# Kernel optimization log

Hardware: AMD Instinct MI355X
Metric: run time of the kernel (lower is better)

The kernel has to match this reference:

```python
import jax, jax.numpy as jnp
import numpy as np

NEG_SLOPE = 0.2


def gat_conv(x, src, dst, W, a_src, a_dst, b, concat):
    # x: [N, F_in], src/dst: [E], W: [F_in, H*C], a_src/a_dst: [H, C], b: [H*C] or [C]
    N = x.shape[0]
    H, C = a_src.shape
    h = (x @ W).reshape(N, H, C)                       # [N, H, C]
    s_src = jnp.sum(h * a_src[None], axis=-1)          # [N, H]
    s_dst = jnp.sum(h * a_dst[None], axis=-1)          # [N, H]
    e = jax.nn.leaky_relu(s_src[src] + s_dst[dst], NEG_SLOPE)  # [E, H]
    m = jax.lax.stop_gradient(jax.ops.segment_max(e, dst, num_segments=N))
    ex = jnp.exp(e - m[dst])                           # [E, H]
    denom = jax.ops.segment_sum(ex, dst, num_segments=N)
    alpha = ex / denom[dst]                            # [E, H]
    msg = h[src] * alpha[:, :, None]                   # [E, H, C]
    out = jax.ops.segment_sum(msg, dst, num_segments=N)  # [N, H, C]
    out = out.reshape(N, H * C) if concat else out.mean(axis=1)
    return out + b


def setup_inputs() -> dict:
    key = jax.random.key(0)
    ks = jax.random.split(key, 10)
    N, E, F_IN, HID, HEADS, OUT = 50000, 1600000, 128, 16, 4, 2
    x = jax.random.normal(ks[0], (N, F_IN), dtype=jnp.float32)
    edge_index = jax.random.randint(ks[1], (2, E), 0, N, dtype=jnp.int32)
    W1 = jax.random.normal(ks[2], (F_IN, HEADS * HID), dtype=jnp.float32) / np.sqrt(F_IN)
    att_src1 = jax.random.normal(ks[3], (HEADS, HID), dtype=jnp.float32) / np.sqrt(HID)
    att_dst1 = jax.random.normal(ks[4], (HEADS, HID), dtype=jnp.float32) / np.sqrt(HID)
    b1 = jnp.zeros((HEADS * HID,), dtype=jnp.float32)
    W2 = jax.random.normal(ks[5], (HEADS * HID, OUT), dtype=jnp.float32) / np.sqrt(HEADS * HID)
    att_src2 = jax.random.normal(ks[6], (1, OUT), dtype=jnp.float32)
    att_dst2 = jax.random.normal(ks[7], (1, OUT), dtype=jnp.float32)
    b2 = jnp.zeros((OUT,), dtype=jnp.float32)
    return {"x": x, "edge_index": edge_index, "W1": W1, "att_src1": att_src1,
            "att_dst1": att_dst1, "b1": b1, "W2": W2, "att_src2": att_src2,
            "att_dst2": att_dst2, "b2": b2}


def reference(x, edge_index, W1, att_src1, att_dst1, b1, W2, att_src2, att_dst2, b2):
    N = x.shape[0]
    # PyG GATConv default: add self-loops
    loop = jnp.arange(N, dtype=edge_index.dtype)
    src = jnp.concatenate([edge_index[0], loop])
    dst = jnp.concatenate([edge_index[1], loop])
    # dropout layers are identity at inference
    h = gat_conv(x, src, dst, W1, att_src1, att_dst1, b1, concat=True)
    h = jax.nn.elu(h)
    out = gat_conv(h, src, dst, W2, att_src2, att_dst2, b2, concat=False)
    return jax.nn.log_softmax(out, axis=1)
```

## Files before the change

### kernel.cpp

```cpp
#include <hip/hip_runtime.h>
#include <cstdint>
#include <cstddef>


#define NEG_SLOPE 0.2f
#define BIN_CHUNK 4096
#define CAP 8192

__device__ __forceinline__ float leaky(float v) {
    return v >= 0.f ? v : NEG_SLOPE * v;
}
__device__ __forceinline__ float elu1(float v) {
    return v > 0.f ? v : expm1f(v);
}
__device__ __forceinline__ unsigned short f2bf(float f) {
    unsigned u = __float_as_uint(f);
    u += 0x7fffu + ((u >> 16) & 1u);
    return (unsigned short)(u >> 16);
}
__device__ __forceinline__ float bflo(unsigned u) {
    return __uint_as_float(u << 16);
}
__device__ __forceinline__ float bfhi(unsigned u) {
    return __uint_as_float(u & 0xFFFF0000u);
}

__global__ void init_cursor_kernel(int* __restrict__ cur, int NB) {
    int t = threadIdx.x;
    if (t < NB) cur[t] = t * CAP;
}

__global__ __launch_bounds__(256) void bin_kernel(
    const int* __restrict__ src, const int* __restrict__ dst,
    int* __restrict__ cursor, unsigned* __restrict__ binned,
    int E, int Etot, int NB) {
    __shared__ int hist[512];
    __shared__ int basesh[512];
    for (int i = threadIdx.x; i < NB; i += 256) hist[i] = 0;
    __syncthreads();
    unsigned pk[BIN_CHUNK / 256];
    int base = blockIdx.x * BIN_CHUNK;
#pragma unroll
    for (int k = 0; k < BIN_CHUNK / 256; ++k) {
        int e = base + k * 256 + threadIdx.x;
        pk[k] = 0xFFFFFFFFu;
        if (e < Etot) {
            int s, d;
            if (e < E) { s = src[e]; d = dst[e]; }
            else       { s = d = e - E; }
            pk[k] = ((unsigned)d << 16) | (unsigned)s;
            atomicAdd(&hist[d >> 7], 1);
        }
    }
    __syncthreads();
    for (int i = threadIdx.x; i < NB; i += 256) {
        int c = hist[i];
        basesh[i] = c ? atomicAdd(&cursor[i], c) : 0;
        hist[i] = 0;
    }
    __syncthreads();
#pragma unroll
    for (int k = 0; k < BIN_CHUNK / 256; ++k) {
        if (pk[k] != 0xFFFFFFFFu) {
            int b = pk[k] >> 23;
            int pos = basesh[b] + atomicAdd(&hist[b], 1);
            binned[pos] = pk[k];
        }
    }
}

__global__ __launch_bounds__(256) void csr_build_kernel(
    const unsigned* __restrict__ binned, const int* __restrict__ cursor,
    int2* __restrict__ rng, int* __restrict__ csr, int N, int NB) {
    __shared__ int hist[128];
    __shared__ int sc[128];
    __shared__ int cur[128];
    const int b = blockIdx.x;
    const int base = b * CAP;
    const int endp = cursor[b];
    const int t = threadIdx.x;
    if (t < 128) hist[t] = 0;
    __syncthreads();
    for (int i = base + t; i < endp; i += 256)
        atomicAdd(&hist[(binned[i] >> 16) & 127], 1);
    __syncthreads();
    int v = (t < 128) ? hist[t] : 0;
    if (t < 128) sc[t] = v;
    __syncthreads();
    for (int off = 1; off < 128; off <<= 1) {
        int u = (t >= off && t < 128) ? sc[t - off] : 0;
        __syncthreads();
        if (t < 128) sc[t] += u;
        __syncthreads();
    }
    if (t < 128) {
        int beg = base + sc[t] - v;
        cur[t] = beg;
        int node = b * 128 + t;
        if (node < N) rng[node] = make_int2(beg, beg + v);
    }
    __syncthreads();
    for (int i = base + t; i < endp; i += 256) {
        unsigned p = binned[i];
        int pos = atomicAdd(&cur[(p >> 16) & 127], 1);
        csr[pos] = (int)(p & 0xFFFFu);
    }
}

__global__ __launch_bounds__(256) void gemm1_kernel(
    const float* __restrict__ x, const float* __restrict__ W1,
    const float* __restrict__ a_src, const float* __restrict__ a_dst,
    unsigned short* __restrict__ h1b, float* __restrict__ ssrc1,
    float* __restrict__ sdst1, int N) {
    __shared__ float Ws[128 * 64];
    __shared__ float Xs[32][129];

    const int t = threadIdx.x;
    const int row0 = blockIdx.x * 32;

    for (int i = t * 4; i < 128 * 64; i += 1024) {
        *(float4*)&Ws[i] = *(const float4*)&W1[i];
    }
    for (int i = t * 4; i < 32 * 128; i += 1024) {
        int r = i >> 7, k = i & 127;
        float4 v = make_float4(0.f, 0.f, 0.f, 0.f);
        if (row0 + r < N) v = *(const float4*)&x[(size_t)(row0 + r) * 128 + k];
        Xs[r][k] = v.x; Xs[r][k + 1] = v.y; Xs[r][k + 2] = v.z; Xs[r][k + 3] = v.w;
    }
    __syncthreads();

    const int r0 = (t >> 4) * 2;
    const int c0 = (t & 15) * 4;
    float a00 = 0.f, a01 = 0.f, a02 = 0.f, a03 = 0.f;
    float a10 = 0.f, a11 = 0.f, a12 = 0.f, a13 = 0.f;
#pragma unroll 8
    for (int k = 0; k < 128; ++k) {
        float4 wv = *(const float4*)&Ws[k * 64 + c0];
        float x0 = Xs[r0][k], x1 = Xs[r0 + 1][k];
        a00 = fmaf(x0, wv.x, a00); a01 = fmaf(x0, wv.y, a01);
        a02 = fmaf(x0, wv.z, a02); a03 = fmaf(x0, wv.w, a03);
        a10 = fmaf(x1, wv.x, a10); a11 = fmaf(x1, wv.y, a11);
        a12 = fmaf(x1, wv.z, a12); a13 = fmaf(x1, wv.w, a13);
    }
    const int rowA = row0 + r0, rowB = rowA + 1;
    if (rowA < N) {
        ushort4 pk;
        pk.x = f2bf(a00); pk.y = f2bf(a01); pk.z = f2bf(a02); pk.w = f2bf(a03);
        *(ushort4*)&h1b[(size_t)rowA * 64 + c0] = pk;
    }
    if (rowB < N) {
        ushort4 pk;
        pk.x = f2bf(a10); pk.y = f2bf(a11); pk.z = f2bf(a12); pk.w = f2bf(a13);
        *(ushort4*)&h1b[(size_t)rowB * 64 + c0] = pk;
    }
    float4 av = *(const float4*)&a_src[c0];
    float4 bv = *(const float4*)&a_dst[c0];
    float ps0 = a00 * av.x + a01 * av.y + a02 * av.z + a03 * av.w;
    float pd0 = a00 * bv.x + a01 * bv.y + a02 * bv.z + a03 * bv.w;
    float ps1 = a10 * av.x + a11 * av.y + a12 * av.z + a13 * av.w;
    float pd1 = a10 * bv.x + a11 * bv.y + a12 * bv.z + a13 * bv.w;
    ps0 += __shfl_xor(ps0, 1); ps0 += __shfl_xor(ps0, 2);
    pd0 += __shfl_xor(pd0, 1); pd0 += __shfl_xor(pd0, 2);
    ps1 += __shfl_xor(ps1, 1); ps1 += __shfl_xor(ps1, 2);
    pd1 += __shfl_xor(pd1, 1); pd1 += __shfl_xor(pd1, 2);
    if ((t & 3) == 0) {
        int head = (t & 15) >> 2;
        if (rowA < N) {
            ssrc1[(size_t)rowA * 4 + head] = ps0;
            sdst1[(size_t)rowA * 4 + head] = pd0;
        }
        if (rowB < N) {
            ssrc1[(size_t)rowB * 4 + head] = ps1;
            sdst1[(size_t)rowB * 4 + head] = pd1;
        }
    }
}

__global__ __launch_bounds__(256) void agg1_kernel(
    const int2* __restrict__ rng, const int* __restrict__ csr,
    const float* __restrict__ ssrc1, const float* __restrict__ sdst1,
    const uint4* __restrict__ h1q,
    const float* __restrict__ b1, const float* __restrict__ W2,
    const float* __restrict__ a_src2, const float* __restrict__ a_dst2,
    float4* __restrict__ pk2, float* __restrict__ sdst2, int N) {
    const int lane = threadIdx.x & 63;
    const int d = blockIdx.x * 4 + (threadIdx.x >> 6);
    if (d >= N) return;
    const int2 r = rng[d];
    const int beg = r.x;
    const int cnt = r.y - r.x;
    const int chl = lane & 7;
    const int sub = lane >> 3;
    const int h = chl >> 1;

    const float bh = sdst1[(size_t)d * 4 + h];

    float acc[8] = {0.f, 0.f, 0.f, 0.f, 0.f, 0.f, 0.f, 0.f};
    float den = 0.f;
    int j = sub;
    for (; j + 8 < cnt; j += 16) {
        int s0 = csr[beg + j];
        int s1 = csr[beg + j + 8];
        float sa0 = ssrc1[(size_t)s0 * 4 + h];
        float sa1 = ssrc1[(size_t)s1 * 4 + h];
        uint4 q0 = h1q[(size_t)s0 * 8 + chl];
        uint4 q1 = h1q[(size_t)s1 * 8 + chl];
        float w0 = __expf(leaky(sa0 + bh));
        float w1 = __expf(leaky(sa1 + bh));
        den += w0 + w1;
        acc[0] = fmaf(w0, bflo(q0.x), acc[0]); acc[1] = fmaf(w0, bfhi(q0.x), acc[1]);
        acc[2] = fmaf(w0, bflo(q0.y), acc[2]); acc[3] = fmaf(w0, bfhi(q0.y), acc[3]);
        acc[4] = fmaf(w0, bflo(q0.z), acc[4]); acc[5] = fmaf(w0, bfhi(q0.z), acc[5]);
        acc[6] = fmaf(w0, bflo(q0.w), acc[6]); acc[7] = fmaf(w0, bfhi(q0.w), acc[7]);
        acc[0] = fmaf(w1, bflo(q1.x), acc[0]); acc[1] = fmaf(w1, bfhi(q1.x), acc[1]);
        acc[2] = fmaf(w1, bflo(q1.y), acc[2]); acc[3] = fmaf(w1, bfhi(q1.y), acc[3]);
        acc[4] = fmaf(w1, bflo(q1.z), acc[4]); acc[5] = fmaf(w1, bfhi(q1.z), acc[5]);
        acc[6] = fmaf(w1, bflo(q1.w), acc[6]); acc[7] = fmaf(w1, bfhi(q1.w), acc[7]);
    }
    if (j < cnt) {
        int s0 = csr[beg + j];
        float sa0 = ssrc1[(size_t)s0 * 4 + h];
        uint4 q0 = h1q[(size_t)s0 * 8 + chl];
        float w0 = __expf(leaky(sa0 + bh));
        den += w0;
        acc[0] = fmaf(w0, bflo(q0.x), acc[0]); acc[1] = fmaf(w0, bfhi(q0.x), acc[1]);
        acc[2] = fmaf(w0, bflo(q0.y), acc[2]); acc[3] = fmaf(w0, bfhi(q0.y), acc[3]);
        acc[4] = fmaf(w0, bflo(q0.z), acc[4]); acc[5] = fmaf(w0, bfhi(q0.z), acc[5]);
        acc[6] = fmaf(w0, bflo(q0.w), acc[6]); acc[7] = fmaf(w0, bfhi(q0.w), acc[7]);
    }
#pragma unroll
    for (int off = 8; off <= 32; off <<= 1) {
        den += __shfl_xor(den, off);
#pragma unroll
        for (int i = 0; i < 8; ++i) acc[i] += __shfl_xor(acc[i], off);
    }
    if (sub == 0) {
        const float inv = 1.f / den;
        const int c = chl * 8;
        float p0 = 0.f, p1 = 0.f;
#pragma unroll
        for (int i = 0; i < 8; ++i) {
            float e = elu1(fmaf(acc[i], inv, 0.f) + b1[c + i]);
            p0 = fmaf(e, W2[(c + i) * 2], p0);
            p1 = fmaf(e, W2[(c + i) * 2 + 1], p1);
        }
        p0 += __shfl_xor(p0, 1); p0 += __shfl_xor(p0, 2); p0 += __shfl_xor(p0, 4);
        p1 += __shfl_xor(p1, 1); p1 += __shfl_xor(p1, 2); p1 += __shfl_xor(p1, 4);
        if (chl == 0) {
            float s2 = p0 * a_src2[0] + p1 * a_src2[1];
            float d2 = p0 * a_dst2[0] + p1 * a_dst2[1];
            pk2[d] = make_float4(p0, p1, s2, 0.f);
            sdst2[d] = d2;
        }
    }
}

__global__ __launch_bounds__(256) void agg2_kernel(
    const int2* __restrict__ rng, const int* __restrict__ csr,
    const float4* __restrict__ pk2, const float* __restrict__ sdst2,
    const float* __restrict__ b2, float* __restrict__ out, int N) {
    const int lane = threadIdx.x & 63;
    const int d = blockIdx.x * 4 + (threadIdx.x >> 6);
    if (d >= N) return;
    const int2 r = rng[d];
    const int beg = r.x;
    const int cnt = r.y - r.x;
    const float bs = sdst2[d];

    float den = 0.f, a0 = 0.f, a1 = 0.f;
    int j = lane;
    for (; j + 64 < cnt; j += 128) {
        int s0 = csr[beg + j];
        int s1 = csr[beg + j + 64];
        float4 p0 = pk2[s0];
        float4 p1 = pk2[s1];
        float w0 = __expf(leaky(p0.z + bs));
        float w1 = __expf(leaky(p1.z + bs));
        den += w0 + w1;
        a0 = fmaf(w0, p0.x, a0); a1 = fmaf(w0, p0.y, a1);
        a0 = fmaf(w1, p1.x, a0); a1 = fmaf(w1, p1.y, a1);
    }
    if (j < cnt) {
        int s0 = csr[beg + j];
        float4 p0 = pk2[s0];
        float w0 = __expf(leaky(p0.z + bs));
        den += w0;
        a0 = fmaf(w0, p0.x, a0); a1 = fmaf(w0, p0.y, a1);
    }
#pragma unroll
    for (int off = 1; off <= 32; off <<= 1) {
        den += __shfl_xor(den, off);
        a0  += __shfl_xor(a0, off);
        a1  += __shfl_xor(a1, off);
    }
    if (lane == 0) {
        float z0 = a0 / den + b2[0];
        float z1 = a1 / den + b2[1];
        float mx = fmaxf(z0, z1);
        float lse = mx + logf(__expf(z0 - mx) + __expf(z1 - mx));
        *(float2*)&out[(size_t)d * 2] = make_float2(z0 - lse, z1 - lse);
    }
}

extern "C" void kernel_launch(void* const* d_in, const int* in_sizes, int n_in,
                              void* d_out, int out_size, void* d_ws, size_t ws_size,
                              hipStream_t stream) {
    const float* x   = (const float*)d_in[0];
    const int*   ei  = (const int*)d_in[1];
    const float* W1  = (const float*)d_in[2];
    const float* as1 = (const float*)d_in[3];
    const float* ad1 = (const float*)d_in[4];
    const float* b1  = (const float*)d_in[5];
    const float* W2  = (const float*)d_in[6];
    const float* as2 = (const float*)d_in[7];
    const float* ad2 = (const float*)d_in[8];
    const float* b2  = (const float*)d_in[9];

    const int N    = in_sizes[0] / 128;
    const int E    = in_sizes[1] / 2;
    const int Etot = E + N;
    const int NB   = (N + 127) >> 7;
    const int* src = ei;
    const int* dst = ei + E;

    char* p = (char*)d_ws;
    float4* pk2 = (float4*)p;           p += (size_t)N * 16;
    unsigned short* h1b = (unsigned short*)p; p += (size_t)N * 64 * 2;
    float* ssrc1 = (float*)p;           p += (size_t)N * 4 * 4;
    float* sdst1 = (float*)p;           p += (size_t)N * 4 * 4;
    float* sdst2 = (float*)p;           p += (size_t)N * 4;
    int2* rng    = (int2*)p;            p += (size_t)N * 8;
    int* cursor  = (int*)p;             p += 512 * 4;
    unsigned* binned = (unsigned*)p;    p += (size_t)NB * CAP * 4;
    int* csr     = (int*)p;             p += (size_t)NB * CAP * 4;

    init_cursor_kernel<<<1, 512, 0, stream>>>(cursor, NB);
    const int nbin = (Etot + BIN_CHUNK - 1) / BIN_CHUNK;
    bin_kernel<<<nbin, 256, 0, stream>>>(src, dst, cursor, binned, E, Etot, NB);
    csr_build_kernel<<<NB, 256, 0, stream>>>(binned, cursor, rng, csr, N, NB);

    gemm1_kernel<<<(N + 31) / 32, 256, 0, stream>>>(x, W1, as1, ad1, h1b, ssrc1, sdst1, N);
    agg1_kernel<<<(N + 3) / 4, 256, 0, stream>>>(rng, csr, ssrc1, sdst1,
                                                 (const uint4*)h1b, b1, W2, as2, ad2,
                                                 pk2, sdst2, N);
    agg2_kernel<<<(N + 3) / 4, 256, 0, stream>>>(rng, csr, pk2, sdst2, b2,
                                                 (float*)d_out, N);
}
```

Baseline: 209.5 us.

## Precompute per-edge fp16 attention weights during CSR build, reorder kernels

Moves the per-edge attention score computation (leaky ReLU plus exp over all four heads) out of the first aggregation kernel and into the CSR build pass, which now runs after the first GEMM. The weights are stored as fp16 in CSR order, so agg1 reads them contiguously instead of gathering ssrc1 per source node and recomputing the exp for each channel lane. The cursor init kernel is replaced by a memset, with bin offsets added in the binning code. The trade-off is an extra edge-sized fp16 buffer that is written once and read back, plus lower precision on the unnormalised weights and a possible fp16 overflow if scores are large.

```diff
diff --git a/kernel.cpp b/kernel.cpp
--- a/kernel.cpp
+++ b/kernel.cpp
@@ -1,4 +1,5 @@
 #include <hip/hip_runtime.h>
+#include <hip/hip_fp16.h>
 #include <cstdint>
 #include <cstddef>
 
@@ -23,11 +24,6 @@
 }
 __device__ __forceinline__ float bfhi(unsigned u) {
     return __uint_as_float(u & 0xFFFF0000u);
-}
-
-__global__ void init_cursor_kernel(int* __restrict__ cur, int NB) {
-    int t = threadIdx.x;
-    if (t < NB) cur[t] = t * CAP;
 }
 
 __global__ __launch_bounds__(256) void bin_kernel(
@@ -55,7 +51,7 @@
     __syncthreads();
     for (int i = threadIdx.x; i < NB; i += 256) {
         int c = hist[i];
-        basesh[i] = c ? atomicAdd(&cursor[i], c) : 0;
+        basesh[i] = c ? (i * CAP + atomicAdd(&cursor[i], c)) : 0;
         hist[i] = 0;
     }
     __syncthreads();
@@ -71,13 +67,15 @@
 
 __global__ __launch_bounds__(256) void csr_build_kernel(
     const unsigned* __restrict__ binned, const int* __restrict__ cursor,
-    int2* __restrict__ rng, int* __restrict__ csr, int N, int NB) {
+    const float* __restrict__ ssrc1, const float* __restrict__ sdst1,
+    int2* __restrict__ rng, int* __restrict__ csr,
+    __half* __restrict__ ew, int N, int NB) {
     __shared__ int hist[128];
     __shared__ int sc[128];
     __shared__ int cur[128];
     const int b = blockIdx.x;
     const int base = b * CAP;
-    const int endp = cursor[b];
+    const int endp = base + cursor[b];
     const int t = threadIdx.x;
     if (t < 128) hist[t] = 0;
     __syncthreads();
@@ -102,8 +100,19 @@
     __syncthreads();
     for (int i = base + t; i < endp; i += 256) {
         unsigned p = binned[i];
-        int pos = atomicAdd(&cur[(p >> 16) & 127], 1);
-        csr[pos] = (int)(p & 0xFFFFu);
+        int node = (p >> 16) & 127;
+        int s = (int)(p & 0xFFFFu);
+        int pos = atomicAdd(&cur[node], 1);
+        csr[pos] = s;
+        int d = b * 128 + node;
+        float4 sa = *(const float4*)&ssrc1[(size_t)s * 4];
+        float4 sd = *(const float4*)&sdst1[(size_t)d * 4];
+        ushort4 wq;
+        wq.x = __half_as_ushort(__float2half(__expf(leaky(sa.x + sd.x))));
+        wq.y = __half_as_ushort(__float2half(__expf(leaky(sa.y + sd.y))));
+        wq.z = __half_as_ushort(__float2half(__expf(leaky(sa.z + sd.z))));
+        wq.w = __half_as_ushort(__float2half(__expf(leaky(sa.w + sd.w))));
+        *(ushort4*)&ew[(size_t)pos * 4] = wq;
     }
 }
 
@@ -178,7 +187,7 @@
 
 __global__ __launch_bounds__(256) void agg1_kernel(
     const int2* __restrict__ rng, const int* __restrict__ csr,
-    const float* __restrict__ ssrc1, const float* __restrict__ sdst1,
+    const __half* __restrict__ ew,
     const uint4* __restrict__ h1q,
     const float* __restrict__ b1, const float* __restrict__ W2,
     const float* __restrict__ a_src2, const float* __restrict__ a_dst2,
@@ -193,20 +202,16 @@
     const int sub = lane >> 3;
     const int h = chl >> 1;
 
-    const float bh = sdst1[(size_t)d * 4 + h];
-
     float acc[8] = {0.f, 0.f, 0.f, 0.f, 0.f, 0.f, 0.f, 0.f};
     float den = 0.f;
     int j = sub;
     for (; j + 8 < cnt; j += 16) {
         int s0 = csr[beg + j];
         int s1 = csr[beg + j + 8];
-        float sa0 = ssrc1[(size_t)s0 * 4 + h];
-        float sa1 = ssrc1[(size_t)s1 * 4 + h];
+        float w0 = __half2float(ew[(size_t)(beg + j) * 4 + h]);
+        float w1 = __half2float(ew[(size_t)(beg + j + 8) * 4 + h]);
         uint4 q0 = h1q[(size_t)s0 * 8 + chl];
         uint4 q1 = h1q[(size_t)s1 * 8 + chl];
-        float w0 = __expf(leaky(sa0 + bh));
-        float w1 = __expf(leaky(sa1 + bh));
         den += w0 + w1;
         acc[0] = fmaf(w0, bflo(q0.x), acc[0]); acc[1] = fmaf(w0, bfhi(q0.x), acc[1]);
         acc[2] = fmaf(w0, bflo(q0.y), acc[2]); acc[3] = fmaf(w0, bfhi(q0.y), acc[3]);
@@ -219,9 +224,8 @@
     }
     if (j < cnt) {
         int s0 = csr[beg + j];
-        float sa0 = ssrc1[(size_t)s0 * 4 + h];
+        float w0 = __half2float(ew[(size_t)(beg + j) * 4 + h]);
         uint4 q0 = h1q[(size_t)s0 * 8 + chl];
-        float w0 = __expf(leaky(sa0 + bh));
         den += w0;
         acc[0] = fmaf(w0, bflo(q0.x), acc[0]); acc[1] = fmaf(w0, bfhi(q0.x), acc[1]);
         acc[2] = fmaf(w0, bflo(q0.y), acc[2]); acc[3] = fmaf(w0, bfhi(q0.y), acc[3]);
@@ -240,7 +244,7 @@
         float p0 = 0.f, p1 = 0.f;
 #pragma unroll
         for (int i = 0; i < 8; ++i) {
-            float e = elu1(fmaf(acc[i], inv, 0.f) + b1[c + i]);
+            float e = elu1(acc[i] * inv + b1[c + i]);
             p0 = fmaf(e, W2[(c + i) * 2], p0);
             p1 = fmaf(e, W2[(c + i) * 2 + 1], p1);
         }
@@ -333,16 +337,17 @@
     int* cursor  = (int*)p;             p += 512 * 4;
     unsigned* binned = (unsigned*)p;    p += (size_t)NB * CAP * 4;
     int* csr     = (int*)p;             p += (size_t)NB * CAP * 4;
-
-    init_cursor_kernel<<<1, 512, 0, stream>>>(cursor, NB);
+    __half* ew   = (__half*)p;          p += (size_t)NB * CAP * 8;
+
+    hipMemsetAsync(cursor, 0, 512 * sizeof(int), stream);
+
     const int nbin = (Etot + BIN_CHUNK - 1) / BIN_CHUNK;
     bin_kernel<<<nbin, 256, 0, stream>>>(src, dst, cursor, binned, E, Etot, NB);
-    csr_build_kernel<<<NB, 256, 0, stream>>>(binned, cursor, rng, csr, N, NB);
-
     gemm1_kernel<<<(N + 31) / 32, 256, 0, stream>>>(x, W1, as1, ad1, h1b, ssrc1, sdst1, N);
-    agg1_kernel<<<(N + 3) / 4, 256, 0, stream>>>(rng, csr, ssrc1, sdst1,
-                                                 (const uint4*)h1b, b1, W2, as2, ad2,
-                                                 pk2, sdst2, N);
+    csr_build_kernel<<<NB, 256, 0, stream>>>(binned, cursor, ssrc1, sdst1,
+                                             rng, csr, ew, N, NB);
+    agg1_kernel<<<(N + 3) / 4, 256, 0, stream>>>(rng, csr, ew, (const uint4*)h1b,
+                                                 b1, W2, as2, ad2, pk2, sdst2, N);
     agg2_kernel<<<(N + 3) / 4, 256, 0, stream>>>(rng, csr, pk2, sdst2, b2,
                                                  (float*)d_out, N);
 }
```

New measurement: 224.4 us. 7.1% more time.
